# Kernel optimization log

Hardware: AMD Instinct MI355X
Metric: run time of the kernel (lower is better)

The kernel has to match this reference:

```python
import jax, jax.numpy as jnp
import numpy as np

HIDDEN = 1024

def setup_inputs() -> dict:
    key = jax.random.key(0)
    ks = jax.random.split(key, 8)
    s = 1.0 / np.sqrt(HIDDEN)
    return {
        "query": jax.random.normal(ks[0], (8, 1024, HIDDEN), dtype=jnp.float32),
        "ref": jax.random.normal(ks[1], (8, 4096, HIDDEN), dtype=jnp.float32),
        "Wq": jax.random.normal(ks[2], (HIDDEN, HIDDEN), dtype=jnp.float32) * s,
        "bq": jax.random.normal(ks[3], (HIDDEN,), dtype=jnp.float32) * s,
        "Wk": jax.random.normal(ks[4], (HIDDEN, HIDDEN), dtype=jnp.float32) * s,
        "bk": jax.random.normal(ks[5], (HIDDEN,), dtype=jnp.float32) * s,
        "Wv": jax.random.normal(ks[6], (HIDDEN, HIDDEN), dtype=jnp.float32) * s,
        "bv": jax.random.normal(ks[7], (HIDDEN,), dtype=jnp.float32) * s,
    }

def reference(query, ref, Wq, bq, Wk, bk, Wv, bv):
    norm_fact = 1.0 / np.sqrt(HIDDEN).astype(np.float32)
    Q = query @ Wq + bq            # [B, Lq, H]
    K = ref @ Wk + bk              # [B, Lk, H]
    V = ref @ Wv + bv              # [B, Lk, H]
    scores = jnp.einsum('bqh,bkh->bqk', Q, K)  # NOTE: unscaled logits (faithful to source)
    attn = jax.nn.softmax(scores, axis=-1) * norm_fact  # post-softmax scale
    return jnp.einsum('bqk,bkh->bqh', attn, V)
```

## Files before the change

### kernel.cpp

```cpp
#include <hip/hip_runtime.h>

typedef _Float16 f16x8 __attribute__((ext_vector_type(8)));
typedef float    f32x4 __attribute__((ext_vector_type(4)));
typedef unsigned short ushort_t;

__device__ __forceinline__ ushort_t f2h(float x) {
    union { _Float16 h; ushort_t u; } c; c.h = (_Float16)x; return c.u;
}

typedef __attribute__((address_space(1))) void gvoid;
typedef __attribute__((address_space(3))) void lvoid;
__device__ __forceinline__ void g2l16(const ushort_t* g, ushort_t* l) {
    __builtin_amdgcn_global_load_lds((gvoid*)g, (lvoid*)l, 16, 0, 0);
}

#define BM 128
#define BN 128
#define BK 32
#define NT 256

__global__ void wconv_kernel(const float* __restrict__ Wq, const float* __restrict__ Wk,
                             const float* __restrict__ Wv,
                             ushort_t* __restrict__ tq, ushort_t* __restrict__ tk,
                             ushort_t* __restrict__ tv) {
    const int z = blockIdx.z;
    const float* W = (z == 0) ? Wq : (z == 1) ? Wk : Wv;
    ushort_t* T = (z == 0) ? tq : (z == 1) ? tk : tv;
    const int n  = blockIdx.x * blockDim.x + threadIdx.x;
    const int kb = blockIdx.y * 128;
    for (int k0 = kb; k0 < kb + 128; k0 += 8) {
        union { ushort_t u[8]; uint4 v; } H;
        #pragma unroll
        for (int e = 0; e < 8; ++e)
            H.u[e] = f2h(W[(long long)(k0 + e) * 1024 + n]);
        *(uint4*)&T[(long long)n * 1024 + k0] = H.v;
    }
}

__global__ void aconv_kernel(const float* __restrict__ x, ushort_t* __restrict__ h, int n4) {
    int i = blockIdx.x * blockDim.x + threadIdx.x;
    if (i >= n4) return;
    float4 v = ((const float4*)x)[i];
    union { ushort_t u[4]; uint2 w; } H;
    H.u[0] = f2h(v.x); H.u[1] = f2h(v.y); H.u[2] = f2h(v.z); H.u[3] = f2h(v.w);
    ((uint2*)h)[i] = H.w;
}

__global__ void add2_kernel(const float4* __restrict__ a, const float4* __restrict__ b,
                            float4* __restrict__ o, int n4) {
    int i = blockIdx.x * blockDim.x + threadIdx.x;
    if (i >= n4) return;
    float4 x = a[i], y = b[i];
    float4 r;
    r.x = x.x + y.x; r.y = x.y + y.y; r.z = x.z + y.z; r.w = x.w + y.w;
    o[i] = r;
}

template<int OUT_MODE, bool BIAS, int NSPLIT>
__global__ __launch_bounds__(NT, 2)
void gemm_kernel(const ushort_t* __restrict__ A, const ushort_t* __restrict__ B,
                 const float* __restrict__ bias,
                 float* __restrict__ Cf, ushort_t* __restrict__ Ch,
                 int K, int lda, int ldb, int ldc,
                 long long sA, long long sB, long long sC, int tM)
{
    __shared__ __align__(16) ushort_t As[BM * BK];
    __shared__ __align__(16) ushort_t Bs[BN * BK];
    __shared__ float biasS[BN];

    const int tid  = threadIdx.x;
    const int zz   = blockIdx.z;
    const int b    = zz / NSPLIT;
    const int kc   = zz % NSPLIT;
    const int m0   = blockIdx.y * BM;
    const int n0   = blockIdx.x * BN;
    const int lane = tid & 63;
    const int w    = tid >> 6;
    const int wm   = (w >> 1) * 64;
    const int wn   = (w & 1) * 64;
    const int l15  = lane & 15;
    const int quad = lane >> 4;

    if (OUT_MODE == 0 && NSPLIT > 1)
        Cf += (long long)kc * (long long)tM;

    if (BIAS && tid < BN) biasS[tid] = bias[n0 + tid];

    const long long aBase = (long long)b * sA + (long long)m0 * lda;
    const long long bBase = (long long)b * sB + (long long)n0 * ldb;

    f32x4 acc[4][4];
    #pragma unroll
    for (int i = 0; i < 4; ++i)
        #pragma unroll
        for (int j = 0; j < 4; ++j)
            #pragma unroll
            for (int r = 0; r < 4; ++r) acc[i][j][r] = 0.0f;

    const int kBeg = kc * K;
    const int kEnd = kBeg + K;
    for (int k0 = kBeg; k0 < kEnd; k0 += BK) {
        __syncthreads();
        {
            const int row = tid >> 2;
            const int col = (tid & 3) * 8;
            const int lds = (tid & ~63) * 8;
            g2l16(A + aBase + (long long)row * lda + k0 + col, &As[lds]);
            g2l16(B + bBase + (long long)row * ldb + k0 + col, &Bs[lds]);
            const int row2 = row + 64;
            const int lds2 = lds + NT * 8;
            g2l16(A + aBase + (long long)row2 * lda + k0 + col, &As[lds2]);
            g2l16(B + bBase + (long long)row2 * ldb + k0 + col, &Bs[lds2]);
        }
        __syncthreads();

        f16x8 af[4], bf[4];
        #pragma unroll
        for (int i = 0; i < 4; ++i)
            af[i] = *(const f16x8*)&As[(wm + i * 16 + l15) * BK + quad * 8];
        #pragma unroll
        for (int j = 0; j < 4; ++j)
            bf[j] = *(const f16x8*)&Bs[(wn + j * 16 + l15) * BK + quad * 8];
        #pragma unroll
        for (int i = 0; i < 4; ++i)
            #pragma unroll
            for (int j = 0; j < 4; ++j)
                acc[i][j] = __builtin_amdgcn_mfma_f32_16x16x32_f16(af[i], bf[j], acc[i][j], 0, 0, 0);
    }

    #pragma unroll
    for (int i = 0; i < 4; ++i)
        #pragma unroll
        for (int j = 0; j < 4; ++j) {
            const int row0 = wm + i * 16 + quad * 4;
            const int col  = wn + j * 16 + l15;
            float c[4];
            #pragma unroll
            for (int r = 0; r < 4; ++r) {
                c[r] = acc[i][j][r];
                if (BIAS) c[r] += biasS[col];
            }
            if constexpr (OUT_MODE == 0) {
                #pragma unroll
                for (int r = 0; r < 4; ++r)
                    Cf[(long long)b * sC + (long long)(m0 + row0 + r) * ldc + (n0 + col)] = c[r];
            } else if constexpr (OUT_MODE == 1) {
                #pragma unroll
                for (int r = 0; r < 4; ++r)
                    Ch[(long long)b * sC + (long long)(m0 + row0 + r) * ldc + (n0 + col)] = f2h(c[r]);
            } else {
                const int mg  = m0 + row0;
                const int bb  = mg / tM;
                const int key = mg % tM;
                union { ushort_t u[4]; uint2 v; } P;
                #pragma unroll
                for (int r = 0; r < 4; ++r) P.u[r] = f2h(c[r]);
                *(uint2*)&Ch[(long long)bb * sC + (long long)(n0 + col) * ldc + key] = P.v;
            }
        }
}

__device__ __forceinline__ f16x8 ldfrag(const ushort_t* base, int row, int ks, int quad) {
    int byte_ = (row << 7) + (ks << 6) + (quad << 4);
    byte_ ^= (row & 7) << 4;
    return *(const f16x8*)((const char*)base + byte_);
}

template<int OUT_MODE, bool BIAS, int NSPLIT>
__global__ __launch_bounds__(512, 2)
void gemm256_kernel(const ushort_t* __restrict__ A, const ushort_t* __restrict__ B,
                    const float* __restrict__ bias,
                    float* __restrict__ Cf, ushort_t* __restrict__ Ch,
                    int K, int lda, int ldb, int ldc,
                    long long sA, long long sB, long long sC, int tM)
{
    __shared__ __align__(16) ushort_t As[2][256 * 64];
    __shared__ __align__(16) ushort_t Bs[2][256 * 64];

    const int tid  = threadIdx.x;
    const int lane = tid & 63;
    const int wid  = tid >> 6;
    const int wr   = wid >> 2;
    const int wc   = wid & 3;
    const int quad = lane >> 4;
    const int l15  = lane & 15;

    const int zz = blockIdx.z;
    const int b  = zz / NSPLIT;
    const int kc = zz % NSPLIT;
    const int m0 = blockIdx.y * 256;
    const int n0 = blockIdx.x * 256;

    const ushort_t* Ab = A + (long long)b * sA + (long long)m0 * lda;
    const ushort_t* Bb = B + (long long)b * sB + (long long)n0 * ldb;

    float* Cfp = Cf;
    if (OUT_MODE == 0 && NSPLIT > 1) Cfp = Cf + (long long)kc * (long long)tM;

    const int NTILES = K >> 6;
    const int kBeg   = kc * K;
    const int tlast  = NTILES - 1;

    const int srow = (wid << 3) + (lane >> 3);
    const int scol = ((lane & 7) ^ ((lane >> 3) & 7)) << 3;

#define STAGE_A(bf, r0, kcol) g2l16(Ab + (long long)((r0) + srow) * lda + (kcol) + scol, \
                                    &As[bf][((r0) + (wid << 3)) << 6])
#define STAGE_B(bf, r0, kcol) g2l16(Bb + (long long)((r0) + srow) * ldb + (kcol) + scol, \
                                    &Bs[bf][((r0) + (wid << 3)) << 6])
#define BAR()  __builtin_amdgcn_s_barrier()
#define SB0()  __builtin_amdgcn_sched_barrier(0)
#define VMCNT(n) asm volatile("s_waitcnt vmcnt(" #n ")" ::: "memory")

    f32x4 acc[8][4];
    #pragma unroll
    for (int i = 0; i < 8; ++i)
        #pragma unroll
        for (int j = 0; j < 4; ++j)
            #pragma unroll
            for (int r = 0; r < 4; ++r) acc[i][j][r] = 0.0f;

    {
        const int k0 = kBeg, k1 = kBeg + 64;
        STAGE_B(0, 0,   k0); STAGE_B(0, 64,  k0);
        STAGE_B(0, 128, k0); STAGE_B(0, 192, k0);
        STAGE_A(0, 0,   k0); STAGE_A(0, 128, k0);
        STAGE_A(0, 64,  k0); STAGE_A(0, 192, k0);
        STAGE_B(1, 0,   k1); STAGE_B(1, 64,  k1);
        STAGE_B(1, 128, k1); STAGE_B(1, 192, k1);
        STAGE_A(1, 0,   k1); STAGE_A(1, 128, k1);
        VMCNT(8);
        BAR(); SB0();
    }

    const int arow = wr * 128 + l15;
    const int brow = wc * 64 + l15;
    f16x8 bfr[4][2], afr[2][2];

#define PHASE_AFR(bf, q) \
    afr[0][0] = ldfrag(&As[bf][0], arow + (q)*32,      0, quad); \
    afr[0][1] = ldfrag(&As[bf][0], arow + (q)*32,      1, quad); \
    afr[1][0] = ldfrag(&As[bf][0], arow + (q)*32 + 16, 0, quad); \
    afr[1][1] = ldfrag(&As[bf][0], arow + (q)*32 + 16, 1, quad);

#define PHASE_MFMA(q) \
    _Pragma("unroll") \
    for (int m2 = 0; m2 < 2; ++m2) \
        _Pragma("unroll") \
        for (int j = 0; j < 4; ++j) { \
            acc[(q)*2+m2][j] = __builtin_amdgcn_mfma_f32_16x16x32_f16(afr[m2][0], bfr[j][0], acc[(q)*2+m2][j], 0, 0, 0); \
            acc[(q)*2+m2][j] = __builtin_amdgcn_mfma_f32_16x16x32_f16(afr[m2][1], bfr[j][1], acc[(q)*2+m2][j], 0, 0, 0); \
        }

#define TILE_BODY(bf, kn1, kn2) { \
     \
    _Pragma("unroll") \
    for (int j = 0; j < 4; ++j) { \
        bfr[j][0] = ldfrag(&Bs[bf][0], brow + j*16, 0, quad); \
        bfr[j][1] = ldfrag(&Bs[bf][0], brow + j*16, 1, quad); \
    } \
    PHASE_AFR(bf, 0); \
    STAGE_A((bf) ^ 1, 64, kn1); STAGE_A((bf) ^ 1, 192, kn1); \
    BAR(); __builtin_amdgcn_s_setprio(1); \
    PHASE_MFMA(0); \
    __builtin_amdgcn_s_setprio(0); BAR(); SB0(); \
     \
    PHASE_AFR(bf, 1); \
    STAGE_B(bf, 0, kn2); STAGE_B(bf, 64, kn2); \
    BAR(); __builtin_amdgcn_s_setprio(1); \
    PHASE_MFMA(1); \
    __builtin_amdgcn_s_setprio(0); VMCNT(10); BAR(); SB0(); \
     \
    PHASE_AFR(bf, 2); \
    STAGE_B(bf, 128, kn2); STAGE_B(bf, 192, kn2); \
    BAR(); __builtin_amdgcn_s_setprio(1); \
    PHASE_MFMA(2); \
    __builtin_amdgcn_s_setprio(0); BAR(); SB0(); \
     \
    PHASE_AFR(bf, 3); \
    STAGE_A(bf, 0, kn2); STAGE_A(bf, 128, kn2); \
    BAR(); __builtin_amdgcn_s_setprio(1); \
    PHASE_MFMA(3); \
    __builtin_amdgcn_s_setprio(0); VMCNT(8); BAR(); SB0(); \
}

    for (int t = 0; t < NTILES; t += 2) {
        {
            const int kn1 = kBeg + (((t + 1) < NTILES ? (t + 1) : tlast) << 6);
            const int kn2 = kBeg + (((t + 2) < NTILES ? (t + 2) : tlast) << 6);
            TILE_BODY(0, kn1, kn2);
        }
        {
            const int kn1 = kBeg + (((t + 2) < NTILES ? (t + 2) : tlast) << 6);
            const int kn2 = kBeg + (((t + 3) < NTILES ? (t + 3) : tlast) << 6);
            TILE_BODY(1, kn1, kn2);
        }
    }

    VMCNT(0);

    float biasv[4];
    if (BIAS) {
        #pragma unroll
        for (int j = 0; j < 4; ++j)
            biasv[j] = bias[n0 + wc * 64 + j * 16 + l15];
    }

    #pragma unroll
    for (int mi = 0; mi < 8; ++mi) {
        const int row0 = wr * 128 + mi * 16 + quad * 4;
        #pragma unroll
        for (int j = 0; j < 4; ++j) {
            const int col = wc * 64 + j * 16 + l15;
            float c[4];
            #pragma unroll
            for (int r = 0; r < 4; ++r) {
                c[r] = acc[mi][j][r];
                if (BIAS) c[r] += biasv[j];
            }
            if constexpr (OUT_MODE == 0) {
                #pragma unroll
                for (int r = 0; r < 4; ++r)
                    Cfp[(long long)b * sC + (long long)(m0 + row0 + r) * ldc + (n0 + col)] = c[r];
            } else if constexpr (OUT_MODE == 1) {
                #pragma unroll
                for (int r = 0; r < 4; ++r)
                    Ch[(long long)b * sC + (long long)(m0 + row0 + r) * ldc + (n0 + col)] = f2h(c[r]);
            } else {
                const int mg  = m0 + row0;
                const int bb2 = mg / tM;
                const int key = mg % tM;
                union { ushort_t u[4]; uint2 v; } Pp;
                #pragma unroll
                for (int r = 0; r < 4; ++r) Pp.u[r] = f2h(c[r]);
                *(uint2*)&Ch[(long long)bb2 * sC + (long long)(n0 + col) * ldc + key] = Pp.v;
            }
        }
    }
#undef STAGE_A
#undef STAGE_B
#undef BAR
#undef SB0
#undef VMCNT
#undef PHASE_AFR
#undef PHASE_MFMA
#undef TILE_BODY
}

__global__ void softmax_kernel(const float* __restrict__ S, ushort_t* __restrict__ P) {
    const int row  = blockIdx.x;
    const int tid  = threadIdx.x;
    const int lane = tid & 63;
    const int wid  = tid >> 6;
    const float* s = S + (long long)row * 4096;
    float4 v[4];
    float m = -3.4e38f;
    #pragma unroll
    for (int i = 0; i < 4; ++i) {
        v[i] = ((const float4*)s)[tid + i * 256];
        m = fmaxf(fmaxf(fmaxf(m, v[i].x), fmaxf(v[i].y, v[i].z)), v[i].w);
    }
    __shared__ float redm[4], reds[4];
    #pragma unroll
    for (int o = 32; o > 0; o >>= 1) m = fmaxf(m, __shfl_down(m, o));
    if (lane == 0) redm[wid] = m;
    __syncthreads();
    m = fmaxf(fmaxf(redm[0], redm[1]), fmaxf(redm[2], redm[3]));
    float sum = 0.f;
    #pragma unroll
    for (int i = 0; i < 4; ++i) {
        v[i].x = __expf(v[i].x - m); v[i].y = __expf(v[i].y - m);
        v[i].z = __expf(v[i].z - m); v[i].w = __expf(v[i].w - m);
        sum += v[i].x + v[i].y + v[i].z + v[i].w;
    }
    #pragma unroll
    for (int o = 32; o > 0; o >>= 1) sum += __shfl_down(sum, o);
    if (lane == 0) reds[wid] = sum;
    __syncthreads();
    sum = reds[0] + reds[1] + reds[2] + reds[3];
    const float scale = 0.03125f / sum;
    ushort_t* p = P + (long long)row * 4096;
    #pragma unroll
    for (int i = 0; i < 4; ++i) {
        union { ushort_t u[4]; uint2 w; } Pk;
        Pk.u[0] = f2h(v[i].x * scale); Pk.u[1] = f2h(v[i].y * scale);
        Pk.u[2] = f2h(v[i].z * scale); Pk.u[3] = f2h(v[i].w * scale);
        ((uint2*)p)[tid + i * 256] = Pk.w;
    }
}

extern "C" void kernel_launch(void* const* d_in, const int* in_sizes, int n_in,
                              void* d_out, int out_size, void* d_ws, size_t ws_size,
                              hipStream_t stream) {
    const float* query = (const float*)d_in[0];
    const float* ref   = (const float*)d_in[1];
    const float* Wq    = (const float*)d_in[2];
    const float* bq    = (const float*)d_in[3];
    const float* Wk    = (const float*)d_in[4];
    const float* bk    = (const float*)d_in[5];
    const float* Wv    = (const float*)d_in[6];
    const float* bv    = (const float*)d_in[7];
    float* out = (float*)d_out;
    (void)in_sizes; (void)n_in; (void)out_size; (void)ws_size;

    char* ws = (char*)d_ws;
    float*    S   = (float*)ws;
    ushort_t* Qa  = (ushort_t*)ws;
    ushort_t* Ra  = (ushort_t*)(ws + 16777216);
    ushort_t* Qp  = (ushort_t*)(ws + 134217728);
    ushort_t* Kp  = (ushort_t*)(ws + 150994944);
    ushort_t* Vt  = (ushort_t*)(ws + 218103808);
    ushort_t* WqT = (ushort_t*)(ws + 282066944);
    ushort_t* WkT = (ushort_t*)(ws + 284164096);
    ushort_t* WvT = (ushort_t*)(ws + 286261248);
    ushort_t* P   = Kp;
    float*    Ppart = (float*)ws;

    wconv_kernel<<<dim3(4, 8, 3), 256, 0, stream>>>(Wq, Wk, Wv, WqT, WkT, WvT);
    aconv_kernel<<<8192, 256, 0, stream>>>(query, Qa, 2097152);
    aconv_kernel<<<32768, 256, 0, stream>>>(ref, Ra, 8388608);

    gemm_kernel<1, true, 1><<<dim3(8, 64, 1), NT, 0, stream>>>(
        Qa, WqT, bq, nullptr, Qp, 1024, 1024, 1024, 1024, 0, 0, 0, 0);
    gemm256_kernel<1, true, 1><<<dim3(4, 128, 1), 512, 0, stream>>>(
        Ra, WkT, bk, nullptr, Kp, 1024, 1024, 1024, 1024, 0, 0, 0, 0);
    gemm256_kernel<3, true, 1><<<dim3(4, 128, 1), 512, 0, stream>>>(
        Ra, WvT, bv, nullptr, Vt, 1024, 1024, 1024, 4096, 0, 0, 4194304LL, 4096);

    gemm256_kernel<0, false, 1><<<dim3(16, 4, 8), 512, 0, stream>>>(
        Qp, Kp, nullptr, S, nullptr, 1024, 1024, 1024, 4096,
        1048576LL, 4194304LL, 4194304LL, 0);

    softmax_kernel<<<8192, 256, 0, stream>>>(S, P);

    gemm256_kernel<0, false, 2><<<dim3(4, 4, 16), 512, 0, stream>>>(
        P, Vt, nullptr, Ppart, nullptr, 2048, 4096, 4096, 1024,
        4194304LL, 4194304LL, 1048576LL, 8388608);

    add2_kernel<<<8192, 256, 0, stream>>>(
        (const float4*)Ppart, (const float4*)(Ppart + 8388608), (float4*)out, 2097152);
}
```

Baseline: 640.0 us.

## Software-pipeline LDS fragment reads ahead of MFMA phases in GEMM main loop

Restructures the GEMM tile loop so each MFMA phase runs on fragments already loaded, while the next phase's A fragments (and the next buffer's B fragments) are read from LDS right after. Removes the scheduling barriers and half of the block barriers, and changes the vmcnt waits and staging order. The aim is to hide LDS read latency behind matrix instructions and cut barrier stalls. It risks hazards where a buffer is overwritten while still being read, and it raises register pressure from prefetched fragments.

```diff
diff --git a/kernel.cpp b/kernel.cpp
--- a/kernel.cpp
+++ b/kernel.cpp
@@ -209,7 +209,8 @@
 #define STAGE_B(bf, r0, kcol) g2l16(Bb + (long long)((r0) + srow) * ldb + (kcol) + scol, \
                                     &Bs[bf][((r0) + (wid << 3)) << 6])
 #define BAR()  __builtin_amdgcn_s_barrier()
-#define SB0()  __builtin_amdgcn_sched_barrier(0)
+#define SETP1  __builtin_amdgcn_s_setprio(1)
+#define SETP0  __builtin_amdgcn_s_setprio(0)
 #define VMCNT(n) asm volatile("s_waitcnt vmcnt(" #n ")" ::: "memory")
 
     f32x4 acc[8][4];
@@ -219,6 +220,32 @@
         for (int j = 0; j < 4; ++j)
             #pragma unroll
             for (int r = 0; r < 4; ++r) acc[i][j][r] = 0.0f;
+
+    const int arow = wr * 128 + l15;
+    const int brow = wc * 64 + l15;
+    f16x8 bfr[4][2], afr[2][2];
+
+#define PHASE_AFR(bf, q) \
+    afr[0][0] = ldfrag(&As[bf][0], arow + (q)*32,      0, quad); \
+    afr[0][1] = ldfrag(&As[bf][0], arow + (q)*32,      1, quad); \
+    afr[1][0] = ldfrag(&As[bf][0], arow + (q)*32 + 16, 0, quad); \
+    afr[1][1] = ldfrag(&As[bf][0], arow + (q)*32 + 16, 1, quad);
+
+#define READS_B(bf) \
+    _Pragma("unroll") \
+    for (int j = 0; j < 4; ++j) { \
+        bfr[j][0] = ldfrag(&Bs[bf][0], brow + j*16, 0, quad); \
+        bfr[j][1] = ldfrag(&Bs[bf][0], brow + j*16, 1, quad); \
+    }
+
+#define PHASE_MFMA(q) \
+    _Pragma("unroll") \
+    for (int m2 = 0; m2 < 2; ++m2) \
+        _Pragma("unroll") \
+        for (int j = 0; j < 4; ++j) { \
+            acc[(q)*2+m2][j] = __builtin_amdgcn_mfma_f32_16x16x32_f16(afr[m2][0], bfr[j][0], acc[(q)*2+m2][j], 0, 0, 0); \
+            acc[(q)*2+m2][j] = __builtin_amdgcn_mfma_f32_16x16x32_f16(afr[m2][1], bfr[j][1], acc[(q)*2+m2][j], 0, 0, 0); \
+        }
 
     {
         const int k0 = kBeg, k1 = kBeg + 64;
@@ -230,58 +257,33 @@
         STAGE_B(1, 128, k1); STAGE_B(1, 192, k1);
         STAGE_A(1, 0,   k1); STAGE_A(1, 128, k1);
         VMCNT(8);
-        BAR(); SB0();
-    }
-
-    const int arow = wr * 128 + l15;
-    const int brow = wc * 64 + l15;
-    f16x8 bfr[4][2], afr[2][2];
-
-#define PHASE_AFR(bf, q) \
-    afr[0][0] = ldfrag(&As[bf][0], arow + (q)*32,      0, quad); \
-    afr[0][1] = ldfrag(&As[bf][0], arow + (q)*32,      1, quad); \
-    afr[1][0] = ldfrag(&As[bf][0], arow + (q)*32 + 16, 0, quad); \
-    afr[1][1] = ldfrag(&As[bf][0], arow + (q)*32 + 16, 1, quad);
-
-#define PHASE_MFMA(q) \
-    _Pragma("unroll") \
-    for (int m2 = 0; m2 < 2; ++m2) \
-        _Pragma("unroll") \
-        for (int j = 0; j < 4; ++j) { \
-            acc[(q)*2+m2][j] = __builtin_amdgcn_mfma_f32_16x16x32_f16(afr[m2][0], bfr[j][0], acc[(q)*2+m2][j], 0, 0, 0); \
-            acc[(q)*2+m2][j] = __builtin_amdgcn_mfma_f32_16x16x32_f16(afr[m2][1], bfr[j][1], acc[(q)*2+m2][j], 0, 0, 0); \
-        }
+        BAR();
+        READS_B(0);
+        PHASE_AFR(0, 0);
+    }
 
 #define TILE_BODY(bf, kn1, kn2) { \
      \
-    _Pragma("unroll") \
-    for (int j = 0; j < 4; ++j) { \
-        bfr[j][0] = ldfrag(&Bs[bf][0], brow + j*16, 0, quad); \
-        bfr[j][1] = ldfrag(&Bs[bf][0], brow + j*16, 1, quad); \
-    } \
-    PHASE_AFR(bf, 0); \
+    SETP1; PHASE_MFMA(0); SETP0; \
+    PHASE_AFR(bf, 1); \
     STAGE_A((bf) ^ 1, 64, kn1); STAGE_A((bf) ^ 1, 192, kn1); \
-    BAR(); __builtin_amdgcn_s_setprio(1); \
-    PHASE_MFMA(0); \
-    __builtin_amdgcn_s_setprio(0); BAR(); SB0(); \
+    VMCNT(8); BAR(); \
      \
-    PHASE_AFR(bf, 1); \
+    SETP1; PHASE_MFMA(1); SETP0; \
+    PHASE_AFR(bf, 2); \
     STAGE_B(bf, 0, kn2); STAGE_B(bf, 64, kn2); \
-    BAR(); __builtin_amdgcn_s_setprio(1); \
-    PHASE_MFMA(1); \
-    __builtin_amdgcn_s_setprio(0); VMCNT(10); BAR(); SB0(); \
+    BAR(); \
      \
-    PHASE_AFR(bf, 2); \
+    SETP1; PHASE_MFMA(2); SETP0; \
+    PHASE_AFR(bf, 3); \
     STAGE_B(bf, 128, kn2); STAGE_B(bf, 192, kn2); \
-    BAR(); __builtin_amdgcn_s_setprio(1); \
-    PHASE_MFMA(2); \
-    __builtin_amdgcn_s_setprio(0); BAR(); SB0(); \
+    STAGE_A(bf, 0, kn2); STAGE_A(bf, 128, kn2); \
+    VMCNT(8); BAR(); \
      \
-    PHASE_AFR(bf, 3); \
-    STAGE_A(bf, 0, kn2); STAGE_A(bf, 128, kn2); \
-    BAR(); __builtin_amdgcn_s_setprio(1); \
-    PHASE_MFMA(3); \
-    __builtin_amdgcn_s_setprio(0); VMCNT(8); BAR(); SB0(); \
+    SETP1; PHASE_MFMA(3); SETP0; \
+    READS_B((bf) ^ 1); \
+    PHASE_AFR((bf) ^ 1, 0); \
+    BAR(); \
 }
 
     for (int t = 0; t < NTILES; t += 2) {
@@ -340,9 +342,11 @@
 #undef STAGE_A
 #undef STAGE_B
 #undef BAR
-#undef SB0
+#undef SETP1
+#undef SETP0
 #undef VMCNT
 #undef PHASE_AFR
+#undef READS_B
 #undef PHASE_MFMA
 #undef TILE_BODY
 }
```

New measurement: 644.2 us. About the same (+0.7%).
